# Optimization experiments

Measured on AMD Instinct MI355X. Metric: run time of the kernel, lower is better.

## Reference

```python
import jax, jax.numpy as jnp
import numpy as np

S_MIN, S_MAX, ALPHA = 1, 5, 5.0
EPS = 1e-6


def _conv2d_same(x, k):
    # x: [B,1,H,W], k: [1,1,3,3], stride 1, padding 1
    return jax.lax.conv_general_dilated(x, k, (1, 1), ((1, 1), (1, 1)),
                                        dimension_numbers=('NCHW', 'OIHW', 'NCHW'))


def sobel_complexity(x):
    # compute_spatial_complexity_sobel: per-image min-max normalized gradient magnitude
    xg = x.mean(1, keepdims=True)  # [B,1,H,W]
    sx = jnp.array([[1, 0, -1], [2, 0, -2], [1, 0, -1]], x.dtype).reshape(1, 1, 3, 3)
    sy = jnp.array([[1, 2, 1], [0, 0, 0], [-1, -2, -1]], x.dtype).reshape(1, 1, 3, 3)
    gx = _conv2d_same(xg, sx)
    gy = _conv2d_same(xg, sy)
    mag = jnp.sqrt(gx ** 2 + gy ** 2 + EPS)
    mn = mag.min((2, 3), keepdims=True)
    mx = mag.max((2, 3), keepdims=True)
    rng = mx - mn
    c = jnp.where(rng > 0, (mag - mn) / (rng + EPS), jnp.zeros_like(mag))
    return c[:, 0]  # [B,H,W]


def adaptive_steps(m):
    # adaptive_step_from_complexity, fully vectorized
    B, H, W = m.shape
    avg = jnp.ones((1, 1, 3, 3), m.dtype) / 9.0
    lc = _conv2d_same(m[:, None], avg)[:, 0]  # [B,H,W] local complexity
    hm, wm = H // 2, W // 2
    rc = jnp.stack([m[:, :hm, :wm].mean((1, 2)), m[:, :hm, wm:].mean((1, 2)),
                    m[:, hm:, :wm].mean((1, 2)), m[:, hm:, wm:].mean((1, 2))], axis=1)  # [B,4]
    base = S_MAX - jax.nn.sigmoid(ALPHA * (rc - 0.5)) * (S_MAX - S_MIN)
    base = jnp.round(jnp.clip(base, S_MIN, S_MAX)).astype(jnp.int32)  # [B,4]
    adj = jnp.round(jax.nn.sigmoid(ALPHA * (lc - 0.5)) * 2.0 - 1.0).astype(jnp.int32)  # [B,H,W]
    return jnp.clip(base[:, :, None, None] + adj[:, None], S_MIN, S_MAX)  # [B,4,H,W]


def _visits_lr(step):
    # step: [B,R,L] int. Left-to-right adaptive-step traversal along last axis per row.
    # Returns float mask [B,R,L] of visited positions.
    B, R, L = step.shape
    s = jnp.maximum(step, 1)

    def body(j, _):
        valid = j < L                       # [B,R]
        jc = jnp.minimum(j, L - 1)
        st = jnp.take_along_axis(s, jc[:, :, None], -1)[:, :, 0]
        return jnp.where(valid, j + st, j), (jc, valid)

    _, (jcs, valids) = jax.lax.scan(body, jnp.zeros((B, R), jnp.int32), None, length=L)
    jcs = jnp.moveaxis(jcs, 0, -1)          # [B,R,L]
    valids = jnp.moveaxis(valids, 0, -1)    # [B,R,L]
    bi = jnp.arange(B)[:, None, None]
    ri = jnp.arange(R)[None, :, None]
    vis = jnp.zeros((B, R, L), jnp.float32).at[bi, ri, jcs].add(valids.astype(jnp.float32))
    return (vis > 0).astype(jnp.float32)


def _visits_rl(step):
    # Right-to-left traversal == left-to-right on the mirrored step map, mirrored back.
    return jnp.flip(_visits_lr(jnp.flip(step, -1)), -1)


def _forward(x):
    m = sobel_complexity(x)                 # [B,H,W]
    steps = adaptive_steps(m)               # [B,4,H,W]
    v0 = _visits_lr(steps[:, 0])            # rows, left->right
    v1 = _visits_rl(steps[:, 1])            # rows, right->left
    v2 = jnp.swapaxes(_visits_lr(jnp.swapaxes(steps[:, 2], 1, 2)), 1, 2)  # cols, top->down
    v3 = jnp.swapaxes(_visits_rl(jnp.swapaxes(steps[:, 3], 1, 2)), 1, 2)  # cols, bottom->up
    V = v0 + v1 + v2 + v3                   # [B,H,W] visit counts
    # DirectionalScan followed by DirectionalMerge: output = sum_d x*visit_d / (V + 1e-6)
    return x * (V / (V + 1e-6))[:, None]


def setup_inputs() -> dict:
    key = jax.random.key(0)
    x = jax.random.normal(key, (8, 96, 256, 256), dtype=jnp.float32)
    return {"x": x}


def reference(x):
    return _forward(x)
```

## Files before the change

kernel.cpp:

```cpp
#include <hip/hip_runtime.h>
#include <math.h>

#define BB 8
#define CC 96
#define HH 256
#define WW 256
#define HW (HH*WW)

typedef unsigned long long u64;
typedef float f32x4 __attribute__((ext_vector_type(4)));
typedef u64 u64x2 __attribute__((ext_vector_type(2)));

__global__ void k_mean(const float* __restrict__ x, float* __restrict__ m,
                       unsigned* __restrict__ mn_u, unsigned* __restrict__ mx_u) {
    if (blockIdx.x == 0 && threadIdx.x < 2 * BB) {
        if (threadIdx.x < BB) mn_u[threadIdx.x] = 0x7f800000u;
        else                  mx_u[threadIdx.x - BB] = 0u;
    }
    int blk = blockIdx.x;
    int b = blk >> 8, tile = blk & 255;
    int wv = threadIdx.x >> 6, ln = threadIdx.x & 63;
    int hw4 = tile * 64 + ln;
    const int per = HW / 4;
    const float4* xb = reinterpret_cast<const float4*>(x)
                     + ((size_t)b * CC + wv * 24) * per + hw4;
    double a0 = 0, a1 = 0, a2 = 0, a3 = 0;
#pragma unroll
    for (int c = 0; c < 24; ++c) {
        float4 v = xb[(size_t)c * per];
        a0 += (double)v.x; a1 += (double)v.y; a2 += (double)v.z; a3 += (double)v.w;
    }
    __shared__ double sbuf[4][4][64];
    sbuf[wv][0][ln] = a0; sbuf[wv][1][ln] = a1;
    sbuf[wv][2][ln] = a2; sbuf[wv][3][ln] = a3;
    __syncthreads();
    if (wv == 0) {
        double r0 = sbuf[0][0][ln] + sbuf[1][0][ln] + sbuf[2][0][ln] + sbuf[3][0][ln];
        double r1 = sbuf[0][1][ln] + sbuf[1][1][ln] + sbuf[2][1][ln] + sbuf[3][1][ln];
        double r2 = sbuf[0][2][ln] + sbuf[1][2][ln] + sbuf[2][2][ln] + sbuf[3][2][ln];
        double r3 = sbuf[0][3][ln] + sbuf[1][3][ln] + sbuf[2][3][ln] + sbuf[3][3][ln];
        float4 o;
        o.x = (float)(r0 / 96.0); o.y = (float)(r1 / 96.0);
        o.z = (float)(r2 / 96.0); o.w = (float)(r3 / 96.0);
        reinterpret_cast<float4*>(m)[(size_t)b * per + hw4] = o;
    }
}

__global__ void k_sobel(const float* __restrict__ m, float* __restrict__ mag,
                        unsigned* mn_u, unsigned* mx_u) {
    int row = blockIdx.x;
    int b = row >> 8, h = row & 255, w = threadIdx.x;
    const float* mb = m + (size_t)b * HW;
    auto at = [&](int hh, int ww) -> float {
        if (hh < 0 || hh >= HH || ww < 0 || ww >= WW) return 0.0f;
        return mb[hh * WW + ww];
    };
    float a00 = at(h - 1, w - 1), a01 = at(h - 1, w), a02 = at(h - 1, w + 1);
    float a10 = at(h, w - 1),                         a12 = at(h, w + 1);
    float a20 = at(h + 1, w - 1), a21 = at(h + 1, w), a22 = at(h + 1, w + 1);
    float gx = a00 - a02 + 2.0f * a10 - 2.0f * a12 + a20 - a22;
    float gy = a00 + 2.0f * a01 + a02 - a20 - 2.0f * a21 - a22;
    float mg = sqrtf(gx * gx + gy * gy + 1e-6f);
    mag[row * WW + w] = mg;

    float lmn = mg, lmx = mg;
    for (int off = 32; off; off >>= 1) {
        lmn = fminf(lmn, __shfl_down(lmn, off));
        lmx = fmaxf(lmx, __shfl_down(lmx, off));
    }
    __shared__ float smn[4], smx[4];
    int wv = threadIdx.x >> 6, ln = threadIdx.x & 63;
    if (ln == 0) { smn[wv] = lmn; smx[wv] = lmx; }
    __syncthreads();
    if (threadIdx.x == 0) {
        float bmn = fminf(fminf(smn[0], smn[1]), fminf(smn[2], smn[3]));
        float bmx = fmaxf(fmaxf(smx[0], smx[1]), fmaxf(smx[2], smx[3]));
        atomicMin(&mn_u[b], __float_as_uint(bmn));
        atomicMax(&mx_u[b], __float_as_uint(bmx));
    }
}

__global__ void k_adjpart(const float* __restrict__ mag, const unsigned* __restrict__ mn_u,
                          const unsigned* __restrict__ mx_u, signed char* __restrict__ adj,
                          float* __restrict__ part) {
    int row = blockIdx.x;
    int b = row >> 8, h = row & 255, w = threadIdx.x;
    float mn = __uint_as_float(mn_u[b]);
    float mx = __uint_as_float(mx_u[b]);
    float rng = mx - mn;
    const float* gb = mag + (size_t)b * HW;
    auto cat = [&](int hh, int ww) -> float {
        if (hh < 0 || hh >= HH || ww < 0 || ww >= WW) return 0.0f;
        float mg = gb[hh * WW + ww];
        return (rng > 0.0f) ? (mg - mn) / (rng + 1e-6f) : 0.0f;
    };
    float cc = cat(h, w);

    float r = cc;
    for (int off = 32; off; off >>= 1) r += __shfl_down(r, off);
    __shared__ float s[4];
    int wv = threadIdx.x >> 6, ln = threadIdx.x & 63;
    if (ln == 0) s[wv] = r;
    __syncthreads();
    if (threadIdx.x == 0) {
        part[row * 2 + 0] = s[0] + s[1];
        part[row * 2 + 1] = s[2] + s[3];
    }

    const float w9 = 1.0f / 9.0f;
    float acc = 0.0f;
    acc = fmaf(cat(h - 1, w - 1), w9, acc);
    acc = fmaf(cat(h - 1, w    ), w9, acc);
    acc = fmaf(cat(h - 1, w + 1), w9, acc);
    acc = fmaf(cat(h    , w - 1), w9, acc);
    acc = fmaf(cc,               w9, acc);
    acc = fmaf(cat(h    , w + 1), w9, acc);
    acc = fmaf(cat(h + 1, w - 1), w9, acc);
    acc = fmaf(cat(h + 1, w    ), w9, acc);
    acc = fmaf(cat(h + 1, w + 1), w9, acc);
    float sg = 1.0f / (1.0f + expf(-5.0f * (acc - 0.5f)));
    adj[row * WW + w] = (signed char)(int)rintf(sg * 2.0f - 1.0f);
}

#define SETBIT(j) do { int _j = (j); \
    if (_j < 64) m0 |= 1ull << _j; \
    else if (_j < 128) m1 |= 1ull << (_j - 64); \
    else if (_j < 192) m2 |= 1ull << (_j - 128); \
    else m3 |= 1ull << (_j - 192); } while (0)

__global__ void k_travbase(const signed char* __restrict__ adj, const float* __restrict__ part,
                           u64* __restrict__ masks, u64* __restrict__ colm) {
    int blk = blockIdx.x;
    int dir = blk >> 3, b = blk & 7;
    int t = threadIdx.x;

    __shared__ double sd[128];
    __shared__ int sbs;
    int hlo = (dir >> 1) ? 128 : 0;
    int col = dir & 1;
    if (t < 128) sd[t] = (double)part[((b << 8) + hlo + t) * 2 + col];
    __syncthreads();
    for (int str = 64; str > 0; str >>= 1) {
        if (t < str) sd[t] += sd[t + str];
        __syncthreads();
    }
    if (t == 0) {
        float rc = (float)(sd[0] / 16384.0);
        float sig = 1.0f / (1.0f + expf(-5.0f * (rc - 0.5f)));
        float bsf = 5.0f - sig * 4.0f;
        bsf = fminf(fmaxf(bsf, 1.0f), 5.0f);
        sbs = (int)rintf(bsf);
    }
    __syncthreads();
    int bs = sbs;

    int r = t;
    const signed char* ab = adj + (size_t)b * HW;
    u64 m0 = 0, m1 = 0, m2 = 0, m3 = 0;
    if (dir == 0) {
        int j = 0;
        while (j < WW) { SETBIT(j);
            int st = bs + (int)ab[r * WW + j];
            st = st < 1 ? 1 : (st > 5 ? 5 : st); j += st; }
    } else if (dir == 1) {
        int j = WW - 1;
        while (j >= 0) { SETBIT(j);
            int st = bs + (int)ab[r * WW + j];
            st = st < 1 ? 1 : (st > 5 ? 5 : st); j -= st; }
    } else if (dir == 2) {
        int j = 0;
        while (j < HH) { SETBIT(j);
            int st = bs + (int)ab[j * WW + r];
            st = st < 1 ? 1 : (st > 5 ? 5 : st); j += st; }
    } else {
        int j = HH - 1;
        while (j >= 0) { SETBIT(j);
            int st = bs + (int)ab[j * WW + r];
            st = st < 1 ? 1 : (st > 5 ? 5 : st); j -= st; }
    }
    if (dir < 2) {
        u64* o = masks + (((size_t)dir * BB + b) * 256 + r) * 4;
        o[0] = m0; o[1] = m1; o[2] = m2; o[3] = m3;
    } else {
        u64* ct = colm + (((size_t)(dir - 2) * BB + b) * 4) * 256 + r;
        ct[0 * 256] = m0; ct[1 * 256] = m1; ct[2 * 256] = m2; ct[3 * 256] = m3;
    }
}

__global__ void k_out(const float* __restrict__ x, const u64* __restrict__ masks,
                      const u64* __restrict__ colm, float* __restrict__ out) {
    const int per_img4 = CC * HW / 4;
    const int hw4n = HW / 4;
    int i = blockIdx.x * blockDim.x + threadIdx.x;
    int b = i / per_img4;
    int hw4 = i & (hw4n - 1);
    int h = hw4 >> 6;
    int w0 = (hw4 & 63) << 2;
    int hb = h & 63, hwd = h >> 6;

    u64 q0 = masks[(((size_t)0 * BB + b) * 256 + h) * 4 + (w0 >> 6)];
    u64 q1 = masks[(((size_t)1 * BB + b) * 256 + h) * 4 + (w0 >> 6)];
    const u64* c2 = colm + (((size_t)0 * BB + b) * 4 + hwd) * 256 + w0;
    const u64* c3 = colm + (((size_t)1 * BB + b) * 4 + hwd) * 256 + w0;
    u64x2 c2a = *reinterpret_cast<const u64x2*>(c2);
    u64x2 c2b = *reinterpret_cast<const u64x2*>(c2 + 2);
    u64x2 c3a = *reinterpret_cast<const u64x2*>(c3);
    u64x2 c3b = *reinterpret_cast<const u64x2*>(c3 + 2);
    u64 cw2[4] = { c2a.x, c2a.y, c2b.x, c2b.y };
    u64 cw3[4] = { c3a.x, c3a.y, c3b.x, c3b.y };

    f32x4 sv;
#pragma unroll
    for (int k = 0; k < 4; ++k) {
        int wbit = (w0 & 63) + k;
        int v = (int)((q0 >> wbit) & 1ull) + (int)((q1 >> wbit) & 1ull)
              + (int)((cw2[k] >> hb) & 1ull) + (int)((cw3[k] >> hb) & 1ull);
        float fV = (float)v;
        sv[k] = fV / (fV + 1e-6f);
    }
    f32x4 xv = reinterpret_cast<const f32x4*>(x)[i];
    f32x4 ov = xv * sv;
    __builtin_nontemporal_store(ov, reinterpret_cast<f32x4*>(out) + i);
}

extern "C" void kernel_launch(void* const* d_in, const int* in_sizes, int n_in,
                              void* d_out, int out_size, void* d_ws, size_t ws_size,
                              hipStream_t stream) {
    const float* x = (const float*)d_in[0];
    float* out = (float*)d_out;
    char* ws = (char*)d_ws;

    size_t off = 0;
    float* m     = (float*)(ws + off); off += (size_t)2 * 1024 * 1024;
    float* mag   = (float*)(ws + off); off += (size_t)2 * 1024 * 1024;
    signed char* adj = (signed char*)(ws + off); off += 524288;
    u64* masks   = (u64*)(ws + off); off += 131072;
    u64* colm    = (u64*)(ws + off); off += 131072;
    float* part  = (float*)(ws + off); off += 16384;
    unsigned* mn_u = (unsigned*)(ws + off);
    unsigned* mx_u = mn_u + 8;

    k_mean<<<BB * 256, 256, 0, stream>>>(x, m, mn_u, mx_u);
    k_sobel<<<BB * HH, 256, 0, stream>>>(m, mag, mn_u, mx_u);
    k_adjpart<<<BB * HH, 256, 0, stream>>>(mag, mn_u, mx_u, adj, part);
    k_travbase<<<32, 256, 0, stream>>>(adj, part, masks, colm);
    k_out<<<(BB * CC * HW / 4) / 256, 256, 0, stream>>>(x, masks, colm, out);
}
```

Before: 168.1 us.

## Fuse four preprocessing kernels into one persistent kernel with grid barriers

The mean, Sobel, adjacency/partial-sum and traversal kernels are merged into one persistent kernel of 1024 blocks. The stages are separated by software grid barriers built on atomics and spin-waits, and the barrier counters are cleared with a memset each call. This removes three kernel launches and their gaps, and the Sobel min/max now issues per-wave atomics directly instead of a block reduction. In exchange it adds the cost of the spin barriers, relies on all 1024 blocks being co-resident (four per CU via launch bounds), and adds a memset.

Measured after the change: 621.8 us. +269.9%, slower.

```diff
diff --git a/kernel.cpp b/kernel.cpp
--- a/kernel.cpp
+++ b/kernel.cpp
@@ -6,120 +6,26 @@
 #define HH 256
 #define WW 256
 #define HW (HH*WW)
+#define NBLK 1024
 
 typedef unsigned long long u64;
 typedef float f32x4 __attribute__((ext_vector_type(4)));
 typedef u64 u64x2 __attribute__((ext_vector_type(2)));
 
-__global__ void k_mean(const float* __restrict__ x, float* __restrict__ m,
-                       unsigned* __restrict__ mn_u, unsigned* __restrict__ mx_u) {
-    if (blockIdx.x == 0 && threadIdx.x < 2 * BB) {
-        if (threadIdx.x < BB) mn_u[threadIdx.x] = 0x7f800000u;
-        else                  mx_u[threadIdx.x - BB] = 0u;
-    }
-    int blk = blockIdx.x;
-    int b = blk >> 8, tile = blk & 255;
-    int wv = threadIdx.x >> 6, ln = threadIdx.x & 63;
-    int hw4 = tile * 64 + ln;
-    const int per = HW / 4;
-    const float4* xb = reinterpret_cast<const float4*>(x)
-                     + ((size_t)b * CC + wv * 24) * per + hw4;
-    double a0 = 0, a1 = 0, a2 = 0, a3 = 0;
-#pragma unroll
-    for (int c = 0; c < 24; ++c) {
-        float4 v = xb[(size_t)c * per];
-        a0 += (double)v.x; a1 += (double)v.y; a2 += (double)v.z; a3 += (double)v.w;
-    }
-    __shared__ double sbuf[4][4][64];
-    sbuf[wv][0][ln] = a0; sbuf[wv][1][ln] = a1;
-    sbuf[wv][2][ln] = a2; sbuf[wv][3][ln] = a3;
-    __syncthreads();
-    if (wv == 0) {
-        double r0 = sbuf[0][0][ln] + sbuf[1][0][ln] + sbuf[2][0][ln] + sbuf[3][0][ln];
-        double r1 = sbuf[0][1][ln] + sbuf[1][1][ln] + sbuf[2][1][ln] + sbuf[3][1][ln];
-        double r2 = sbuf[0][2][ln] + sbuf[1][2][ln] + sbuf[2][2][ln] + sbuf[3][2][ln];
-        double r3 = sbuf[0][3][ln] + sbuf[1][3][ln] + sbuf[2][3][ln] + sbuf[3][3][ln];
-        float4 o;
-        o.x = (float)(r0 / 96.0); o.y = (float)(r1 / 96.0);
-        o.z = (float)(r2 / 96.0); o.w = (float)(r3 / 96.0);
-        reinterpret_cast<float4*>(m)[(size_t)b * per + hw4] = o;
-    }
-}
-
-__global__ void k_sobel(const float* __restrict__ m, float* __restrict__ mag,
-                        unsigned* mn_u, unsigned* mx_u) {
-    int row = blockIdx.x;
-    int b = row >> 8, h = row & 255, w = threadIdx.x;
-    const float* mb = m + (size_t)b * HW;
-    auto at = [&](int hh, int ww) -> float {
-        if (hh < 0 || hh >= HH || ww < 0 || ww >= WW) return 0.0f;
-        return mb[hh * WW + ww];
-    };
-    float a00 = at(h - 1, w - 1), a01 = at(h - 1, w), a02 = at(h - 1, w + 1);
-    float a10 = at(h, w - 1),                         a12 = at(h, w + 1);
-    float a20 = at(h + 1, w - 1), a21 = at(h + 1, w), a22 = at(h + 1, w + 1);
-    float gx = a00 - a02 + 2.0f * a10 - 2.0f * a12 + a20 - a22;
-    float gy = a00 + 2.0f * a01 + a02 - a20 - 2.0f * a21 - a22;
-    float mg = sqrtf(gx * gx + gy * gy + 1e-6f);
-    mag[row * WW + w] = mg;
-
-    float lmn = mg, lmx = mg;
-    for (int off = 32; off; off >>= 1) {
-        lmn = fminf(lmn, __shfl_down(lmn, off));
-        lmx = fmaxf(lmx, __shfl_down(lmx, off));
-    }
-    __shared__ float smn[4], smx[4];
-    int wv = threadIdx.x >> 6, ln = threadIdx.x & 63;
-    if (ln == 0) { smn[wv] = lmn; smx[wv] = lmx; }
+__device__ __forceinline__ void gbar(unsigned* cnt, unsigned* flag) {
     __syncthreads();
     if (threadIdx.x == 0) {
-        float bmn = fminf(fminf(smn[0], smn[1]), fminf(smn[2], smn[3]));
-        float bmx = fmaxf(fmaxf(smx[0], smx[1]), fmaxf(smx[2], smx[3]));
-        atomicMin(&mn_u[b], __float_as_uint(bmn));
-        atomicMax(&mx_u[b], __float_as_uint(bmx));
-    }
-}
-
-__global__ void k_adjpart(const float* __restrict__ mag, const unsigned* __restrict__ mn_u,
-                          const unsigned* __restrict__ mx_u, signed char* __restrict__ adj,
-                          float* __restrict__ part) {
-    int row = blockIdx.x;
-    int b = row >> 8, h = row & 255, w = threadIdx.x;
-    float mn = __uint_as_float(mn_u[b]);
-    float mx = __uint_as_float(mx_u[b]);
-    float rng = mx - mn;
-    const float* gb = mag + (size_t)b * HW;
-    auto cat = [&](int hh, int ww) -> float {
-        if (hh < 0 || hh >= HH || ww < 0 || ww >= WW) return 0.0f;
-        float mg = gb[hh * WW + ww];
-        return (rng > 0.0f) ? (mg - mn) / (rng + 1e-6f) : 0.0f;
-    };
-    float cc = cat(h, w);
-
-    float r = cc;
-    for (int off = 32; off; off >>= 1) r += __shfl_down(r, off);
-    __shared__ float s[4];
-    int wv = threadIdx.x >> 6, ln = threadIdx.x & 63;
-    if (ln == 0) s[wv] = r;
+        __threadfence();
+        unsigned v = atomicAdd(cnt, 1u);
+        if (v == NBLK - 1u) {
+            __threadfence();
+            atomicExch(flag, 1u);
+        } else {
+            while (atomicAdd(flag, 0u) == 0u) { __builtin_amdgcn_s_sleep(2); }
+        }
+        __threadfence();
+    }
     __syncthreads();
-    if (threadIdx.x == 0) {
-        part[row * 2 + 0] = s[0] + s[1];
-        part[row * 2 + 1] = s[2] + s[3];
-    }
-
-    const float w9 = 1.0f / 9.0f;
-    float acc = 0.0f;
-    acc = fmaf(cat(h - 1, w - 1), w9, acc);
-    acc = fmaf(cat(h - 1, w    ), w9, acc);
-    acc = fmaf(cat(h - 1, w + 1), w9, acc);
-    acc = fmaf(cat(h    , w - 1), w9, acc);
-    acc = fmaf(cc,               w9, acc);
-    acc = fmaf(cat(h    , w + 1), w9, acc);
-    acc = fmaf(cat(h + 1, w - 1), w9, acc);
-    acc = fmaf(cat(h + 1, w    ), w9, acc);
-    acc = fmaf(cat(h + 1, w + 1), w9, acc);
-    float sg = 1.0f / (1.0f + expf(-5.0f * (acc - 0.5f)));
-    adj[row * WW + w] = (signed char)(int)rintf(sg * 2.0f - 1.0f);
 }
 
 #define SETBIT(j) do { int _j = (j); \
@@ -128,62 +34,171 @@
     else if (_j < 192) m2 |= 1ull << (_j - 128); \
     else m3 |= 1ull << (_j - 192); } while (0)
 
-__global__ void k_travbase(const signed char* __restrict__ adj, const float* __restrict__ part,
-                           u64* __restrict__ masks, u64* __restrict__ colm) {
-    int blk = blockIdx.x;
-    int dir = blk >> 3, b = blk & 7;
-    int t = threadIdx.x;
-
+__global__ __launch_bounds__(256, 4)
+void k_fused(const float* __restrict__ x, float* __restrict__ m, float* __restrict__ mag,
+             signed char* __restrict__ adj, float* __restrict__ part,
+             u64* __restrict__ masks, u64* __restrict__ colm,
+             unsigned* __restrict__ mn_u, unsigned* __restrict__ mx_u,
+             unsigned* __restrict__ bar) {
+    __shared__ double sbuf[4][4][64];
+    __shared__ float s4[4];
     __shared__ double sd[128];
     __shared__ int sbs;
-    int hlo = (dir >> 1) ? 128 : 0;
-    int col = dir & 1;
-    if (t < 128) sd[t] = (double)part[((b << 8) + hlo + t) * 2 + col];
-    __syncthreads();
-    for (int str = 64; str > 0; str >>= 1) {
-        if (t < str) sd[t] += sd[t + str];
-        __syncthreads();
-    }
-    if (t == 0) {
-        float rc = (float)(sd[0] / 16384.0);
-        float sig = 1.0f / (1.0f + expf(-5.0f * (rc - 0.5f)));
-        float bsf = 5.0f - sig * 4.0f;
-        bsf = fminf(fmaxf(bsf, 1.0f), 5.0f);
-        sbs = (int)rintf(bsf);
-    }
-    __syncthreads();
-    int bs = sbs;
-
-    int r = t;
-    const signed char* ab = adj + (size_t)b * HW;
-    u64 m0 = 0, m1 = 0, m2 = 0, m3 = 0;
-    if (dir == 0) {
-        int j = 0;
-        while (j < WW) { SETBIT(j);
-            int st = bs + (int)ab[r * WW + j];
-            st = st < 1 ? 1 : (st > 5 ? 5 : st); j += st; }
-    } else if (dir == 1) {
-        int j = WW - 1;
-        while (j >= 0) { SETBIT(j);
-            int st = bs + (int)ab[r * WW + j];
-            st = st < 1 ? 1 : (st > 5 ? 5 : st); j -= st; }
-    } else if (dir == 2) {
-        int j = 0;
-        while (j < HH) { SETBIT(j);
-            int st = bs + (int)ab[j * WW + r];
-            st = st < 1 ? 1 : (st > 5 ? 5 : st); j += st; }
-    } else {
-        int j = HH - 1;
-        while (j >= 0) { SETBIT(j);
-            int st = bs + (int)ab[j * WW + r];
-            st = st < 1 ? 1 : (st > 5 ? 5 : st); j -= st; }
-    }
-    if (dir < 2) {
-        u64* o = masks + (((size_t)dir * BB + b) * 256 + r) * 4;
-        o[0] = m0; o[1] = m1; o[2] = m2; o[3] = m3;
-    } else {
-        u64* ct = colm + (((size_t)(dir - 2) * BB + b) * 4) * 256 + r;
-        ct[0 * 256] = m0; ct[1 * 256] = m1; ct[2 * 256] = m2; ct[3 * 256] = m3;
+
+    int tid = threadIdx.x, wv = tid >> 6, ln = tid & 63;
+
+    if (blockIdx.x == 0 && tid < 2 * BB) {
+        if (tid < BB) mn_u[tid] = 0x7f800000u;
+        else          mx_u[tid - BB] = 0u;
+    }
+
+    for (int u = blockIdx.x; u < BB * 256; u += NBLK) {
+        int b = u >> 8, tile = u & 255;
+        int hw4 = tile * 64 + ln;
+        const int per = HW / 4;
+        const float4* xb = reinterpret_cast<const float4*>(x)
+                         + ((size_t)b * CC + wv * 24) * per + hw4;
+        double a0 = 0, a1 = 0, a2 = 0, a3 = 0;
+#pragma unroll
+        for (int c = 0; c < 24; ++c) {
+            float4 v = xb[(size_t)c * per];
+            a0 += (double)v.x; a1 += (double)v.y; a2 += (double)v.z; a3 += (double)v.w;
+        }
+        __syncthreads();
+        sbuf[wv][0][ln] = a0; sbuf[wv][1][ln] = a1;
+        sbuf[wv][2][ln] = a2; sbuf[wv][3][ln] = a3;
+        __syncthreads();
+        if (wv == 0) {
+            double r0 = sbuf[0][0][ln] + sbuf[1][0][ln] + sbuf[2][0][ln] + sbuf[3][0][ln];
+            double r1 = sbuf[0][1][ln] + sbuf[1][1][ln] + sbuf[2][1][ln] + sbuf[3][1][ln];
+            double r2 = sbuf[0][2][ln] + sbuf[1][2][ln] + sbuf[2][2][ln] + sbuf[3][2][ln];
+            double r3 = sbuf[0][3][ln] + sbuf[1][3][ln] + sbuf[2][3][ln] + sbuf[3][3][ln];
+            float4 o;
+            o.x = (float)(r0 / 96.0); o.y = (float)(r1 / 96.0);
+            o.z = (float)(r2 / 96.0); o.w = (float)(r3 / 96.0);
+            reinterpret_cast<float4*>(m)[(size_t)b * per + hw4] = o;
+        }
+    }
+    gbar(bar + 0, bar + 1);
+
+    for (int u = blockIdx.x; u < BB * HH; u += NBLK) {
+        int b = u >> 8, h = u & 255, w = tid;
+        const float* mb = m + (size_t)b * HW;
+        auto at = [&](int hh, int ww) -> float {
+            if (hh < 0 || hh >= HH || ww < 0 || ww >= WW) return 0.0f;
+            return mb[hh * WW + ww];
+        };
+        float a00 = at(h - 1, w - 1), a01 = at(h - 1, w), a02 = at(h - 1, w + 1);
+        float a10 = at(h, w - 1),                         a12 = at(h, w + 1);
+        float a20 = at(h + 1, w - 1), a21 = at(h + 1, w), a22 = at(h + 1, w + 1);
+        float gx = a00 - a02 + 2.0f * a10 - 2.0f * a12 + a20 - a22;
+        float gy = a00 + 2.0f * a01 + a02 - a20 - 2.0f * a21 - a22;
+        float mg = sqrtf(gx * gx + gy * gy + 1e-6f);
+        mag[u * WW + w] = mg;
+
+        float lmn = mg, lmx = mg;
+        for (int off = 32; off; off >>= 1) {
+            lmn = fminf(lmn, __shfl_down(lmn, off));
+            lmx = fmaxf(lmx, __shfl_down(lmx, off));
+        }
+        if (ln == 0) {
+            atomicMin(&mn_u[b], __float_as_uint(lmn));
+            atomicMax(&mx_u[b], __float_as_uint(lmx));
+        }
+    }
+    gbar(bar + 2, bar + 3);
+
+    for (int u = blockIdx.x; u < BB * HH; u += NBLK) {
+        int b = u >> 8, h = u & 255, w = tid;
+        float mn = __uint_as_float(mn_u[b]);
+        float mx = __uint_as_float(mx_u[b]);
+        float rng = mx - mn;
+        const float* gb = mag + (size_t)b * HW;
+        auto cat = [&](int hh, int ww) -> float {
+            if (hh < 0 || hh >= HH || ww < 0 || ww >= WW) return 0.0f;
+            float mg = gb[hh * WW + ww];
+            return (rng > 0.0f) ? (mg - mn) / (rng + 1e-6f) : 0.0f;
+        };
+        float cc = cat(h, w);
+
+        float r = cc;
+        for (int off = 32; off; off >>= 1) r += __shfl_down(r, off);
+        __syncthreads();
+        if (ln == 0) s4[wv] = r;
+        __syncthreads();
+        if (tid == 0) {
+            part[u * 2 + 0] = s4[0] + s4[1];
+            part[u * 2 + 1] = s4[2] + s4[3];
+        }
+
+        const float w9 = 1.0f / 9.0f;
+        float acc = 0.0f;
+        acc = fmaf(cat(h - 1, w - 1), w9, acc);
+        acc = fmaf(cat(h - 1, w    ), w9, acc);
+        acc = fmaf(cat(h - 1, w + 1), w9, acc);
+        acc = fmaf(cat(h    , w - 1), w9, acc);
+        acc = fmaf(cc,               w9, acc);
+        acc = fmaf(cat(h    , w + 1), w9, acc);
+        acc = fmaf(cat(h + 1, w - 1), w9, acc);
+        acc = fmaf(cat(h + 1, w    ), w9, acc);
+        acc = fmaf(cat(h + 1, w + 1), w9, acc);
+        float sg = 1.0f / (1.0f + expf(-5.0f * (acc - 0.5f)));
+        adj[u * WW + w] = (signed char)(int)rintf(sg * 2.0f - 1.0f);
+    }
+    gbar(bar + 4, bar + 5);
+
+    if (blockIdx.x < 32) {
+        int dir = blockIdx.x >> 3, b = blockIdx.x & 7;
+        int t = tid;
+        int hlo = (dir >> 1) ? 128 : 0;
+        int col = dir & 1;
+        if (t < 128) sd[t] = (double)part[((b << 8) + hlo + t) * 2 + col];
+        __syncthreads();
+        for (int str = 64; str > 0; str >>= 1) {
+            if (t < str) sd[t] += sd[t + str];
+            __syncthreads();
+        }
+        if (t == 0) {
+            float rc = (float)(sd[0] / 16384.0);
+            float sig = 1.0f / (1.0f + expf(-5.0f * (rc - 0.5f)));
+            float bsf = 5.0f - sig * 4.0f;
+            bsf = fminf(fmaxf(bsf, 1.0f), 5.0f);
+            sbs = (int)rintf(bsf);
+        }
+        __syncthreads();
+        int bs = sbs;
+
+        int r = t;
+        const signed char* ab = adj + (size_t)b * HW;
+        u64 m0 = 0, m1 = 0, m2 = 0, m3 = 0;
+        if (dir == 0) {
+            int j = 0;
+            while (j < WW) { SETBIT(j);
+                int st = bs + (int)ab[r * WW + j];
+                st = st < 1 ? 1 : (st > 5 ? 5 : st); j += st; }
+        } else if (dir == 1) {
+            int j = WW - 1;
+            while (j >= 0) { SETBIT(j);
+                int st = bs + (int)ab[r * WW + j];
+                st = st < 1 ? 1 : (st > 5 ? 5 : st); j -= st; }
+        } else if (dir == 2) {
+            int j = 0;
+            while (j < HH) { SETBIT(j);
+                int st = bs + (int)ab[j * WW + r];
+                st = st < 1 ? 1 : (st > 5 ? 5 : st); j += st; }
+        } else {
+            int j = HH - 1;
+            while (j >= 0) { SETBIT(j);
+                int st = bs + (int)ab[j * WW + r];
+                st = st < 1 ? 1 : (st > 5 ? 5 : st); j -= st; }
+        }
+        if (dir < 2) {
+            u64* o = masks + (((size_t)dir * BB + b) * 256 + r) * 4;
+            o[0] = m0; o[1] = m1; o[2] = m2; o[3] = m3;
+        } else {
+            u64* ct = colm + (((size_t)(dir - 2) * BB + b) * 4) * 256 + r;
+            ct[0 * 256] = m0; ct[1 * 256] = m1; ct[2 * 256] = m2; ct[3 * 256] = m3;
+        }
     }
 }
 
@@ -237,12 +252,11 @@
     u64* masks   = (u64*)(ws + off); off += 131072;
     u64* colm    = (u64*)(ws + off); off += 131072;
     float* part  = (float*)(ws + off); off += 16384;
-    unsigned* mn_u = (unsigned*)(ws + off);
+    unsigned* mn_u = (unsigned*)(ws + off); off += 64;
     unsigned* mx_u = mn_u + 8;
-
-    k_mean<<<BB * 256, 256, 0, stream>>>(x, m, mn_u, mx_u);
-    k_sobel<<<BB * HH, 256, 0, stream>>>(m, mag, mn_u, mx_u);
-    k_adjpart<<<BB * HH, 256, 0, stream>>>(mag, mn_u, mx_u, adj, part);
-    k_travbase<<<32, 256, 0, stream>>>(adj, part, masks, colm);
+    unsigned* bar  = (unsigned*)(ws + off); off += 64;
+
+    hipMemsetAsync(bar, 0, 6 * sizeof(unsigned), stream);
+    k_fused<<<NBLK, 256, 0, stream>>>(x, m, mag, adj, part, masks, colm, mn_u, mx_u, bar);
     k_out<<<(BB * CC * HW / 4) / 256, 256, 0, stream>>>(x, masks, colm, out);
 }
```

## Fuse traversal into adj kernel via last-block ticket; loop channels in output kernel

Applied to the files above, without the earlier changes.

Merges the small traversal kernel into the adjacency kernel. The last 32 blocks to finish take a ticket from an atomic counter, spin until every block has finished, then run the per-direction traversals. This removes one kernel launch and its launch gap. The output kernel now computes the visit scale once per pixel and loops over all 96 channels, instead of recomputing the masks for every channel element. That loop cuts mask-load and index work but leaves far fewer threads for the bandwidth-bound pass, and the spin-wait relies on all blocks being able to make progress.

Result: slower. 316.3 us (+88.2%).

```diff
diff --git a/kernel.cpp b/kernel.cpp
--- a/kernel.cpp
+++ b/kernel.cpp
@@ -12,10 +12,12 @@
 typedef u64 u64x2 __attribute__((ext_vector_type(2)));
 
 __global__ void k_mean(const float* __restrict__ x, float* __restrict__ m,
-                       unsigned* __restrict__ mn_u, unsigned* __restrict__ mx_u) {
-    if (blockIdx.x == 0 && threadIdx.x < 2 * BB) {
-        if (threadIdx.x < BB) mn_u[threadIdx.x] = 0x7f800000u;
-        else                  mx_u[threadIdx.x - BB] = 0u;
+                       unsigned* __restrict__ mn_u, unsigned* __restrict__ mx_u,
+                       unsigned* __restrict__ tcnt) {
+    if (blockIdx.x == 0) {
+        if (threadIdx.x < BB)            mn_u[threadIdx.x] = 0x7f800000u;
+        else if (threadIdx.x < 2 * BB)   mx_u[threadIdx.x - BB] = 0u;
+        else if (threadIdx.x == 2 * BB)  tcnt[0] = 0u;
     }
     int blk = blockIdx.x;
     int b = blk >> 8, tile = blk & 255;
@@ -80,9 +82,17 @@
     }
 }
 
-__global__ void k_adjpart(const float* __restrict__ mag, const unsigned* __restrict__ mn_u,
+#define SETBIT(j) do { int _j = (j); \
+    if (_j < 64) m0 |= 1ull << _j; \
+    else if (_j < 128) m1 |= 1ull << (_j - 64); \
+    else if (_j < 192) m2 |= 1ull << (_j - 128); \
+    else m3 |= 1ull << (_j - 192); } while (0)
+
+__global__ void k_adjtrav(const float* __restrict__ mag, const unsigned* __restrict__ mn_u,
                           const unsigned* __restrict__ mx_u, signed char* __restrict__ adj,
-                          float* __restrict__ part) {
+                          float* __restrict__ part, u64* __restrict__ masks,
+                          u64* __restrict__ colm, unsigned* __restrict__ tcnt) {
+    const unsigned NB = BB * HH;
     int row = blockIdx.x;
     int b = row >> 8, h = row & 255, w = threadIdx.x;
     float mn = __uint_as_float(mn_u[b]);
@@ -120,25 +130,31 @@
     acc = fmaf(cat(h + 1, w + 1), w9, acc);
     float sg = 1.0f / (1.0f + expf(-5.0f * (acc - 0.5f)));
     adj[row * WW + w] = (signed char)(int)rintf(sg * 2.0f - 1.0f);
-}
-
-#define SETBIT(j) do { int _j = (j); \
-    if (_j < 64) m0 |= 1ull << _j; \
-    else if (_j < 128) m1 |= 1ull << (_j - 64); \
-    else if (_j < 192) m2 |= 1ull << (_j - 128); \
-    else m3 |= 1ull << (_j - 192); } while (0)
-
-__global__ void k_travbase(const signed char* __restrict__ adj, const float* __restrict__ part,
-                           u64* __restrict__ masks, u64* __restrict__ colm) {
-    int blk = blockIdx.x;
-    int dir = blk >> 3, b = blk & 7;
+
+    __threadfence();
+    __syncthreads();
+    __shared__ unsigned stkt;
+    if (threadIdx.x == 0) stkt = atomicAdd(tcnt, 1u);
+    __syncthreads();
+    unsigned tkt = stkt;
+    if (tkt < NB - 32u) return;
+
+    if (threadIdx.x == 0) {
+        while (__hip_atomic_load(tcnt, __ATOMIC_RELAXED, __HIP_MEMORY_SCOPE_AGENT) < NB)
+            __builtin_amdgcn_s_sleep(1);
+    }
+    __syncthreads();
+    __threadfence();
+
+    int unit = (int)(tkt - (NB - 32u));
+    int dir = unit >> 3, tb = unit & 7;
     int t = threadIdx.x;
 
     __shared__ double sd[128];
     __shared__ int sbs;
     int hlo = (dir >> 1) ? 128 : 0;
     int col = dir & 1;
-    if (t < 128) sd[t] = (double)part[((b << 8) + hlo + t) * 2 + col];
+    if (t < 128) sd[t] = (double)part[((tb << 8) + hlo + t) * 2 + col];
     __syncthreads();
     for (int str = 64; str > 0; str >>= 1) {
         if (t < str) sd[t] += sd[t + str];
@@ -154,46 +170,45 @@
     __syncthreads();
     int bs = sbs;
 
-    int r = t;
-    const signed char* ab = adj + (size_t)b * HW;
+    int rr = t;
+    const signed char* ab = adj + (size_t)tb * HW;
     u64 m0 = 0, m1 = 0, m2 = 0, m3 = 0;
     if (dir == 0) {
         int j = 0;
         while (j < WW) { SETBIT(j);
-            int st = bs + (int)ab[r * WW + j];
+            int st = bs + (int)ab[rr * WW + j];
             st = st < 1 ? 1 : (st > 5 ? 5 : st); j += st; }
     } else if (dir == 1) {
         int j = WW - 1;
         while (j >= 0) { SETBIT(j);
-            int st = bs + (int)ab[r * WW + j];
+            int st = bs + (int)ab[rr * WW + j];
             st = st < 1 ? 1 : (st > 5 ? 5 : st); j -= st; }
     } else if (dir == 2) {
         int j = 0;
         while (j < HH) { SETBIT(j);
-            int st = bs + (int)ab[j * WW + r];
+            int st = bs + (int)ab[j * WW + rr];
             st = st < 1 ? 1 : (st > 5 ? 5 : st); j += st; }
     } else {
         int j = HH - 1;
         while (j >= 0) { SETBIT(j);
-            int st = bs + (int)ab[j * WW + r];
+            int st = bs + (int)ab[j * WW + rr];
             st = st < 1 ? 1 : (st > 5 ? 5 : st); j -= st; }
     }
     if (dir < 2) {
-        u64* o = masks + (((size_t)dir * BB + b) * 256 + r) * 4;
+        u64* o = masks + (((size_t)dir * BB + tb) * 256 + rr) * 4;
         o[0] = m0; o[1] = m1; o[2] = m2; o[3] = m3;
     } else {
-        u64* ct = colm + (((size_t)(dir - 2) * BB + b) * 4) * 256 + r;
+        u64* ct = colm + (((size_t)(dir - 2) * BB + tb) * 4) * 256 + rr;
         ct[0 * 256] = m0; ct[1 * 256] = m1; ct[2 * 256] = m2; ct[3 * 256] = m3;
     }
 }
 
 __global__ void k_out(const float* __restrict__ x, const u64* __restrict__ masks,
                       const u64* __restrict__ colm, float* __restrict__ out) {
-    const int per_img4 = CC * HW / 4;
-    const int hw4n = HW / 4;
+    const int per = HW / 4;
     int i = blockIdx.x * blockDim.x + threadIdx.x;
-    int b = i / per_img4;
-    int hw4 = i & (hw4n - 1);
+    int b = i >> 14;
+    int hw4 = i & (per - 1);
     int h = hw4 >> 6;
     int w0 = (hw4 & 63) << 2;
     int hb = h & 63, hwd = h >> 6;
@@ -218,9 +233,14 @@
         float fV = (float)v;
         sv[k] = fV / (fV + 1e-6f);
     }
-    f32x4 xv = reinterpret_cast<const f32x4*>(x)[i];
-    f32x4 ov = xv * sv;
-    __builtin_nontemporal_store(ov, reinterpret_cast<f32x4*>(out) + i);
+
+    const f32x4* xb = reinterpret_cast<const f32x4*>(x) + (size_t)b * CC * per + hw4;
+    f32x4* ob = reinterpret_cast<f32x4*>(out) + (size_t)b * CC * per + hw4;
+#pragma unroll 4
+    for (int c = 0; c < CC; ++c) {
+        f32x4 xv = xb[(size_t)c * per];
+        __builtin_nontemporal_store(xv * sv, ob + (size_t)c * per);
+    }
 }
 
 extern "C" void kernel_launch(void* const* d_in, const int* in_sizes, int n_in,
@@ -237,12 +257,12 @@
     u64* masks   = (u64*)(ws + off); off += 131072;
     u64* colm    = (u64*)(ws + off); off += 131072;
     float* part  = (float*)(ws + off); off += 16384;
-    unsigned* mn_u = (unsigned*)(ws + off);
+    unsigned* mn_u = (unsigned*)(ws + off); off += 64;
     unsigned* mx_u = mn_u + 8;
-
-    k_mean<<<BB * 256, 256, 0, stream>>>(x, m, mn_u, mx_u);
+    unsigned* tcnt = (unsigned*)(ws + off); off += 64;
+
+    k_mean<<<BB * 256, 256, 0, stream>>>(x, m, mn_u, mx_u, tcnt);
     k_sobel<<<BB * HH, 256, 0, stream>>>(m, mag, mn_u, mx_u);
-    k_adjpart<<<BB * HH, 256, 0, stream>>>(mag, mn_u, mx_u, adj, part);
-    k_travbase<<<32, 256, 0, stream>>>(adj, part, masks, colm);
-    k_out<<<(BB * CC * HW / 4) / 256, 256, 0, stream>>>(x, masks, colm, out);
-}
+    k_adjtrav<<<BB * HH, 256, 0, stream>>>(mag, mn_u, mx_u, adj, part, masks, colm, tcnt);
+    k_out<<<(BB * HW / 4) / 256, 256, 0, stream>>>(x, masks, colm, out);
+}
```
